# Optimization experiments

Hardware: AMD Instinct MI355X
Metric: run time of the kernel (lower is better)

Reference implementation:

```python
import jax, jax.numpy as jnp
import numpy as np

N_HEAD = 16
ROPE_BASE = 10000.0


def _rope_cache(T, head_dim):
    # half-split RoPE: cos/sin of shape [T, head_dim//2]
    half = head_dim // 2
    inv_freq = ROPE_BASE ** (-jnp.arange(half, dtype=jnp.float32) / half)
    angles = jnp.arange(T, dtype=jnp.float32)[:, None] * inv_freq[None, :]  # [T, half]
    return jnp.cos(angles), jnp.sin(angles)


def _apply_rope(x, cos, sin):
    # x: [B, H, T, D]; cos/sin: [T, D//2]
    half = x.shape[-1] // 2
    x1, x2 = x[..., :half], x[..., half:]
    c = cos[None, None, :, :]
    s = sin[None, None, :, :]
    return jnp.concatenate([x1 * c - x2 * s, x1 * s + x2 * c], axis=-1)


def setup_inputs() -> dict:
    key = jax.random.key(0)
    k1, k2, k3 = jax.random.split(key, 3)
    B, T, C = 2, 2048, 1024
    x = jax.random.normal(k1, (B, T, C), dtype=jnp.float32)
    w_attn = jax.random.normal(k2, (C, 3 * C), dtype=jnp.float32) * (C ** -0.5)
    b_attn = jnp.zeros((3 * C,), dtype=jnp.float32)
    w_proj = jax.random.normal(k3, (C, C), dtype=jnp.float32) * (C ** -0.5)
    b_proj = jnp.zeros((C,), dtype=jnp.float32)
    return {"x": x, "w_attn": w_attn, "b_attn": b_attn, "w_proj": w_proj, "b_proj": b_proj}


def reference(x, w_attn, b_attn, w_proj, b_proj):
    B, T, C = x.shape
    H = N_HEAD
    hd = C // H

    qkv = x @ w_attn + b_attn                      # [B, T, 3C] fused QKV
    q, k, v = jnp.split(qkv, 3, axis=-1)
    q = q.reshape(B, T, H, hd).transpose(0, 2, 1, 3)  # [B, H, T, hd]
    k = k.reshape(B, T, H, hd).transpose(0, 2, 1, 3)
    v = v.reshape(B, T, H, hd).transpose(0, 2, 1, 3)

    cos, sin = _rope_cache(T, hd)
    q = _apply_rope(q, cos, sin)
    k = _apply_rope(k, cos, sin)

    scale = 1.0 / jnp.sqrt(jnp.float32(hd))
    att = jnp.einsum("bhqd,bhkd->bhqk", q, k) * scale  # [B, H, T, T]
    causal = jnp.tril(jnp.ones((T, T), dtype=bool))
    att = jnp.where(causal[None, None], att, -jnp.inf)
    att = jax.nn.softmax(att, axis=-1)
    y = jnp.einsum("bhqk,bhkd->bhqd", att, v)          # [B, H, T, hd]
    y = y.transpose(0, 2, 1, 3).reshape(B, T, C)
    return y @ w_proj + b_proj
```

## Files before the change

kernel.cpp:

```cpp
#include <hip/hip_runtime.h>
#include <hip/hip_bf16.h>
#include <cmath>

typedef _Float16 half_t;
typedef half_t half4 __attribute__((ext_vector_type(4)));
typedef half_t half8 __attribute__((ext_vector_type(8)));
typedef float f32x4 __attribute__((ext_vector_type(4)));

#define N_HEADS 16
#define HD      64
#define T_SEQ   2048
#define B_SZ    2
#define C_DIM   1024
#define M_ROWS  (B_SZ * T_SEQ)
#define N_QKV   (3 * C_DIM)
#define QSCALE  0.18033688f

__device__ inline void load_lds16(const half_t* g, half_t* l) {
  __builtin_amdgcn_global_load_lds(
      (const __attribute__((address_space(1))) void*)g,
      (__attribute__((address_space(3))) void*)l, 16, 0, 0);
}

__global__ __launch_bounds__(256) void k_prep(const float* __restrict__ x,
                                              half_t* __restrict__ xb,
                                              const float* __restrict__ wa,
                                              half_t* __restrict__ wT,
                                              const float* __restrict__ wp,
                                              half_t* __restrict__ wpT,
                                              float2* __restrict__ tbl) {
  __shared__ float tile[64][65];
  int bid = blockIdx.x, tid = threadIdx.x;
  if (bid < 4096) {
    int i = (bid * 256 + tid) * 4;
    float4 v = *(const float4*)(x + i);
    half_t o[4] = {(half_t)v.x, (half_t)v.y, (half_t)v.z, (half_t)v.w};
    *(ulong1*)(xb + i) = *(ulong1*)o;
    return;
  }
  if (bid >= 5120) {
    int idx = (bid - 5120) * 256 + tid;
    int t = idx >> 5, j = idx & 31;
    float inv = exp2f(-(float)j * (13.287712379549449f / 32.0f));
    float s, c;
    sincosf((float)t * inv, &s, &c);
    tbl[idx] = make_float2(c, s);
    return;
  }
  const float* in; half_t* out; int K, N, id;
  if (bid < 4864) { id = bid - 4096; in = wa; out = wT;  K = 1024; N = 3072; }
  else            { id = bid - 4864; in = wp; out = wpT; K = 1024; N = 1024; }
  int n0 = (id % (N / 64)) * 64, k0 = (id / (N / 64)) * 64;
  int tx = tid & 63, ty = tid >> 6;
  #pragma unroll
  for (int i = 0; i < 64; i += 4)
    tile[ty + i][tx] = in[(size_t)(k0 + ty + i) * N + n0 + tx];
  __syncthreads();
  #pragma unroll
  for (int i = 0; i < 64; i += 4) {
    int r = ty + i;
    out[(size_t)(n0 + r) * K + k0 + tx] = (half_t)tile[tx][r];
  }
}

template <typename OT, int TN>
__global__ __launch_bounds__(256) void k_gemm(const half_t* __restrict__ A,
                                              const half_t* __restrict__ Bt,
                                              const float* __restrict__ bias,
                                              OT* __restrict__ C,
                                              int M, int N, int K) {
  constexpr int NI = TN / 32;
  __shared__ half_t As[2][128 * 64];
  __shared__ half_t Bs[2][TN * 64];
  int tid = threadIdx.x;
  int wave = tid >> 6, lane = tid & 63;
  int lane15 = lane & 15, quad = lane >> 4;
  int wm = (wave >> 1) * 64, wn = (wave & 1) * (TN / 2);
  int bm0 = blockIdx.y * 128, bn0 = blockIdx.x * TN;
  f32x4 acc[4][NI] = {};

#define G_STAGE(bb, kb)                                                        \
  {                                                                            \
    const half_t* Ag = A + (size_t)bm0 * K + (kb);                             \
    const half_t* Bg = Bt + (size_t)bn0 * K + (kb);                            \
    _Pragma("unroll")                                                          \
    for (int p = 0; p < 4; p++) {                                              \
      int fc = wave * 4 * 64 + p * 64 + lane;                                  \
      int r = fc >> 3, c = (fc & 7) ^ (r & 7);                                 \
      load_lds16(Ag + (size_t)r * K + c * 8, &As[bb][0] + (wave * 4 + p) * 512); \
    }                                                                          \
    _Pragma("unroll")                                                          \
    for (int p = 0; p < NI; p++) {                                             \
      int fc = wave * NI * 64 + p * 64 + lane;                                 \
      int r = fc >> 3, c = (fc & 7) ^ (r & 7);                                 \
      load_lds16(Bg + (size_t)r * K + c * 8, &Bs[bb][0] + (wave * NI + p) * 512); \
    }                                                                          \
  }

  G_STAGE(0, 0);
  int NT = K / 64;
  for (int kt = 0; kt < NT; kt++) {
    __syncthreads();
    if (kt + 1 < NT) G_STAGE((kt + 1) & 1, (kt + 1) * 64);
    const half_t* Asb = &As[kt & 1][0];
    const half_t* Bsb = &Bs[kt & 1][0];
    #pragma unroll
    for (int ks = 0; ks < 2; ks++) {
      half8 af[4], bf[NI];
      #pragma unroll
      for (int i = 0; i < 4; i++) {
        int Ra = wm + i * 16 + lane15;
        af[i] = *(const half8*)(Asb + Ra * 64 + ((ks * 4 + quad) ^ (Ra & 7)) * 8);
      }
      #pragma unroll
      for (int i = 0; i < NI; i++) {
        int Rb = wn + i * 16 + lane15;
        bf[i] = *(const half8*)(Bsb + Rb * 64 + ((ks * 4 + quad) ^ (Rb & 7)) * 8);
      }
      #pragma unroll
      for (int mi = 0; mi < 4; mi++)
        #pragma unroll
        for (int ni = 0; ni < NI; ni++)
          acc[mi][ni] = __builtin_amdgcn_mfma_f32_16x16x32_f16(af[mi], bf[ni], acc[mi][ni], 0, 0, 0);
    }
  }
#undef G_STAGE
  #pragma unroll
  for (int mi = 0; mi < 4; mi++)
    #pragma unroll
    for (int ni = 0; ni < NI; ni++) {
      int n = bn0 + wn + ni * 16 + lane15;
      float bv = bias[n];
      int mrow = bm0 + wm + mi * 16 + quad * 4;
      #pragma unroll
      for (int r = 0; r < 4; r++)
        C[(size_t)(mrow + r) * N + n] = (OT)(acc[mi][ni][r] + bv);
    }
}

__global__ __launch_bounds__(256) void k_gemm_qkv(const half_t* __restrict__ A,
                                                  const half_t* __restrict__ Bt,
                                                  const float* __restrict__ bias,
                                                  const float2* __restrict__ tbl,
                                                  half_t* __restrict__ Qo,
                                                  half_t* __restrict__ Ko,
                                                  half_t* __restrict__ Vo) {
  __shared__ half_t smem[2][16384];
  int tid = threadIdx.x;
  int wave = tid >> 6, lane = tid & 63;
  int lane15 = lane & 15, quad = lane >> 4;
  int wm = (wave >> 1) * 64, wn = (wave & 1) * 64;
  int bm0 = blockIdx.y * 128, bn0 = blockIdx.x * 128;
  f32x4 acc[4][4] = {};

#define QKV_STAGE(bb, kb)                                                      \
  {                                                                            \
    const half_t* Ag = A + (size_t)bm0 * C_DIM + (kb);                         \
    const half_t* Bg = Bt + (size_t)bn0 * C_DIM + (kb);                        \
    _Pragma("unroll")                                                          \
    for (int p = 0; p < 4; p++) {                                              \
      int fc = wave * 4 * 64 + p * 64 + lane;                                  \
      int r = fc >> 3, c = (fc & 7) ^ (r & 7);                                 \
      load_lds16(Ag + (size_t)r * C_DIM + c * 8,                               \
                 &smem[bb][0] + (wave * 4 + p) * 512);                         \
      load_lds16(Bg + (size_t)r * C_DIM + c * 8,                               \
                 &smem[bb][8192] + (wave * 4 + p) * 512);                      \
    }                                                                          \
  }

  QKV_STAGE(0, 0);
  for (int kt = 0; kt < 16; kt++) {
    __syncthreads();
    if (kt < 15) QKV_STAGE((kt + 1) & 1, (kt + 1) * 64);
    const half_t* As = &smem[kt & 1][0];
    const half_t* Bs = &smem[kt & 1][8192];
    #pragma unroll
    for (int ks = 0; ks < 2; ks++) {
      half8 af[4], bf[4];
      #pragma unroll
      for (int i = 0; i < 4; i++) {
        int Ra = wm + i * 16 + lane15;
        af[i] = *(const half8*)(As + Ra * 64 + ((ks * 4 + quad) ^ (Ra & 7)) * 8);
      }
      #pragma unroll
      for (int i = 0; i < 4; i++) {
        int Rb = wn + i * 16 + lane15;
        bf[i] = *(const half8*)(Bs + Rb * 64 + ((ks * 4 + quad) ^ (Rb & 7)) * 8);
      }
      #pragma unroll
      for (int mi = 0; mi < 4; mi++)
        #pragma unroll
        for (int ni = 0; ni < 4; ni++)
          acc[mi][ni] = __builtin_amdgcn_mfma_f32_16x16x32_f16(af[mi], bf[ni], acc[mi][ni], 0, 0, 0);
    }
  }
#undef QKV_STAGE
  #pragma unroll
  for (int ni = 0; ni < 4; ni++) {
    float bv = bias[bn0 + wn + ni * 16 + lane15];
    #pragma unroll
    for (int mi = 0; mi < 4; mi++)
      #pragma unroll
      for (int r = 0; r < 4; r++) acc[mi][ni][r] += bv;
  }

  int third = bn0 >> 10;
  if (third < 2) {
    half_t* Ob = (third == 0) ? Qo : Ko;
    int h = ((bn0 & 1023) + wn) >> 6;
    #pragma unroll
    for (int mi = 0; mi < 4; mi++) {
      int mrow = bm0 + wm + mi * 16 + quad * 4;
      int bq = mrow >> 11, tq = mrow & 2047;
      half_t* outp = Ob + ((size_t)(bq * 16 + h) * T_SEQ + tq) * HD;
      #pragma unroll
      for (int p = 0; p < 2; p++) {
        int j = p * 16 + lane15;
        #pragma unroll
        for (int r = 0; r < 4; r++) {
          float2 cs = tbl[(tq + r) * 32 + j];
          float a1 = acc[mi][p][r], a2 = acc[mi][p + 2][r];
          float o1 = a1 * cs.x - a2 * cs.y;
          float o2 = a1 * cs.y + a2 * cs.x;
          if (third == 0) { o1 *= QSCALE; o2 *= QSCALE; }
          outp[r * HD + j]      = (half_t)o1;
          outp[r * HD + j + 32] = (half_t)o2;
        }
      }
    }
  } else {
    __syncthreads();
    half_t* vt = &smem[0][0];
    #pragma unroll
    for (int mi = 0; mi < 4; mi++)
      #pragma unroll
      for (int ni = 0; ni < 4; ni++) {
        int tl = wm + mi * 16 + quad * 4, nl = wn + ni * 16 + lane15;
        #pragma unroll
        for (int r = 0; r < 4; r++)
          vt[(tl + r) * 130 + nl] = (half_t)acc[mi][ni][r];
      }
    __syncthreads();
    int hV = (bn0 - 2048) >> 6;
    int bq = bm0 >> 11, tq0 = bm0 & 2047;
    int c8 = (tid & 7) * 8;
    #pragma unroll
    for (int p = 0; p < 8; p++) {
      int gr = p * 32 + (tid >> 3);
      int tb = gr & 1, d = (gr >> 1) & 63, h2 = gr >> 7;
      half8 vv;
      #pragma unroll
      for (int jj = 0; jj < 8; jj++)
        vv[jj] = vt[(tb * 64 + c8 + jj) * 130 + h2 * 64 + d];
      *(half8*)(Vo + ((size_t)((bq * 16 + hV + h2) * 32 + (tq0 >> 6) + tb) * 64 + d) * 64 + c8) = vv;
    }
  }
}

template <bool DIAG>
__device__ __forceinline__ void tile_mfma(const half_t* __restrict__ Kt,
                                          const half_t* __restrict__ Vt,
                                          half8 bq0, half8 bq1,
                                          f32x4 (&ot)[4], float& l,
                                          int lane15, int quad, int qloc) {
  f32x4 sacc[4];
  #pragma unroll
  for (int s = 0; s < 4; s++) {
    int R_ = s * 16 + lane15;
    half8 ak0 = *(const half8*)(Kt + R_ * 64 + ((quad) ^ (R_ & 7)) * 8);
    half8 ak1 = *(const half8*)(Kt + R_ * 64 + ((4 + quad) ^ (R_ & 7)) * 8);
    f32x4 z = {};
    z = __builtin_amdgcn_mfma_f32_16x16x32_f16(ak0, bq0, z, 0, 0, 0);
    sacc[s] = __builtin_amdgcn_mfma_f32_16x16x32_f16(ak1, bq1, z, 0, 0, 0);
  }
  #pragma unroll
  for (int s = 0; s < 4; s++) {
    half4 bp;
    #pragma unroll
    for (int r = 0; r < 4; r++) {
      float sv = sacc[s][r];
      if (DIAG && (s * 16 + quad * 4 + r > qloc)) sv = -1.0e30f;
      float p = exp2f(fminf(sv, 14.0f));
      l += p;
      bp[r] = (half_t)p;
    }
    #pragma unroll
    for (int nm = 0; nm < 4; nm++) {
      int Rv = nm * 16 + lane15;
      half4 av = *(const half4*)(Vt + Rv * 64 +
                                 ((2 * s + (quad >> 1)) ^ (Rv & 7)) * 8 +
                                 (quad & 1) * 4);
      ot[nm] = __builtin_amdgcn_mfma_f32_16x16x16f16(av, bp, ot[nm], 0, 0, 0);
    }
  }
}

#define STAGE(bb, t_)                                                          \
  {                                                                            \
    int gS = wave >> 3;                                                        \
    int idx = (wave & 7) * 64 + lane;                                          \
    int rr_ = idx >> 3, cc = (idx & 7) ^ (rr_ & 7);                            \
    int j = 2 * (t_) + gS;                                                     \
    load_lds16(Kb + (size_t)(j * 64 + rr_) * HD + cc * 8,                      \
               &KV[bb][0][gS][0] + idx * 8);                                   \
    load_lds16(Vb + (size_t)j * 4096 + rr_ * 64 + cc * 8,                      \
               &KV[bb][1][gS][0] + idx * 8);                                   \
  }

__device__ __forceinline__ void process_tile(
    int qt, const half_t* __restrict__ Qb, const half_t* __restrict__ Kb,
    const half_t* __restrict__ Vb, half_t* __restrict__ y, int b, int h,
    half_t (&KV)[2][2][2][4096],
    int wave, int lane, int g, int wq, int lane15, int quad) {
  int q0 = qt * 128;
  int qrow = q0 + wq * 16 + lane15;
  half8 bq0 = *(const half8*)(Qb + (size_t)qrow * HD + quad * 8);
  half8 bq1 = *(const half8*)(Qb + (size_t)qrow * HD + 32 + quad * 8);
  f32x4 ot[4] = {};
  float l = 0.f;
  int R = qt + 1;
  for (int r = 0; r < R - 1; r++) {
    __syncthreads();
    STAGE((r + 1) & 1, r + 1);
    tile_mfma<false>(&KV[r & 1][0][g][0], &KV[r & 1][1][g][0], bq0, bq1, ot, l,
                     lane15, quad, 0);
  }
  __syncthreads();
  {
    int buf = (R - 1) & 1;
    const half_t* Kt = &KV[buf][0][g][0];
    const half_t* Vt = &KV[buf][1][g][0];
    if (g == 0)
      tile_mfma<true>(Kt, Vt, bq0, bq1, ot, l, lane15, quad, wq * 16 + lane15);
    else if (wq >= 4)
      tile_mfma<true>(Kt, Vt, bq0, bq1, ot, l, lane15, quad,
                      (wq - 4) * 16 + lane15);
  }
  l += __shfl_xor(l, 16);
  l += __shfl_xor(l, 32);
  __syncthreads();
  float* cb = (float*)&KV[0][0][0][0];
  int ci = (wq * 64 + lane) * 17;
  if (g == 1) {
    #pragma unroll
    for (int nm = 0; nm < 4; nm++)
      #pragma unroll
      for (int r = 0; r < 4; r++) cb[ci + nm * 4 + r] = ot[nm][r];
    cb[ci + 16] = l;
  }
  __syncthreads();
  if (g == 0) {
    #pragma unroll
    for (int nm = 0; nm < 4; nm++)
      #pragma unroll
      for (int r = 0; r < 4; r++) ot[nm][r] += cb[ci + nm * 4 + r];
    l += cb[ci + 16];
    float invl = 1.0f / l;
    int t = q0 + wq * 16 + lane15;
    half_t* yr = y + (size_t)(b * T_SEQ + t) * C_DIM + h * 64;
    #pragma unroll
    for (int nm = 0; nm < 4; nm++) {
      half4 o4;
      #pragma unroll
      for (int r = 0; r < 4; r++) o4[r] = (half_t)(ot[nm][r] * invl);
      *(half4*)(yr + nm * 16 + quad * 4) = o4;
    }
  }
  __syncthreads();
}

__global__ __launch_bounds__(1024, 4) void k_flash(const half_t* __restrict__ Qg,
                                                   const half_t* __restrict__ Kg,
                                                   const half_t* __restrict__ Vg,
                                                   half_t* __restrict__ y) {
  __shared__ half_t KV[2][2][2][4096];
  int bh = blockIdx.y;
  int b = bh >> 4, h = bh & 15;
  int x = blockIdx.x;
  int tid = threadIdx.x;
  int wave = tid >> 6, lane = tid & 63;
  int g = wave >> 3, wq = wave & 7;
  int lane15 = lane & 15, quad = lane >> 4;
  const half_t* Qb = Qg + (size_t)bh * T_SEQ * HD;
  const half_t* Kb = Kg + (size_t)bh * T_SEQ * HD;
  const half_t* Vb = Vg + (size_t)bh * HD * T_SEQ;

  int qtA = x, qtB = 15 - x;
  STAGE(0, 0);
  process_tile(qtA, Qb, Kb, Vb, y, b, h, KV, wave, lane, g, wq, lane15, quad);
  STAGE(0, 0);
  process_tile(qtB, Qb, Kb, Vb, y, b, h, KV, wave, lane, g, wq, lane15, quad);
  #undef STAGE
}

extern "C" void kernel_launch(void* const* d_in, const int* in_sizes, int n_in,
                              void* d_out, int out_size, void* d_ws, size_t ws_size,
                              hipStream_t stream) {
  const float* x      = (const float*)d_in[0];
  const float* w_attn = (const float*)d_in[1];
  const float* b_attn = (const float*)d_in[2];
  const float* w_proj = (const float*)d_in[3];
  const float* b_proj = (const float*)d_in[4];
  float* out = (float*)d_out;

  char* ws = (char*)d_ws;
  const size_t MB = 1u << 20;
  half_t* xb  = (half_t*)(ws);
  half_t* wT  = (half_t*)(ws + 8 * MB);
  half_t* wpT = (half_t*)(ws + 14 * MB);
  half_t* Q   = (half_t*)(ws + 16 * MB);
  half_t* Kb  = (half_t*)(ws + 24 * MB);
  half_t* Vt  = (half_t*)(ws + 32 * MB);
  half_t* y   = (half_t*)(ws + 40 * MB);
  float2* tbl = (float2*)(ws + 48 * MB);

  k_prep<<<4096 + 768 + 256 + 256, 256, 0, stream>>>(x, xb, w_attn, wT,
                                                     w_proj, wpT, tbl);
  k_gemm_qkv<<<dim3(N_QKV / 128, M_ROWS / 128), 256, 0, stream>>>(
      xb, wT, b_attn, tbl, Q, Kb, Vt);
  k_flash<<<dim3(8, B_SZ * N_HEADS), 1024, 0, stream>>>(Q, Kb, Vt, y);
  k_gemm<float, 64><<<dim3(C_DIM / 64, M_ROWS / 128), 256, 0, stream>>>(
      y, wpT, b_proj, out, M_ROWS, C_DIM, C_DIM);
}
```

Measured before the change: 184.2 us.

## Share K/V tile loads across paired query tiles and remap block indices

The flash kernel used to handle its two query tiles (x and 15-x) one after the other, restaging K/V from the start for the second tile. It now runs a single loop over the longer tile's K/V range and applies each staged K/V tile to both query blocks, so the shared prefix is loaded and synchronized once. Block indices are also remapped so that consecutive blocks cover different heads. The cost is a second set of accumulators per wave, which raises register pressure and may lower occupancy under the 1024-thread launch bound.

```diff
diff --git a/kernel.cpp b/kernel.cpp
--- a/kernel.cpp
+++ b/kernel.cpp
@@ -307,76 +307,15 @@
                &KV[bb][1][gS][0] + idx * 8);                                   \
   }
 
-__device__ __forceinline__ void process_tile(
-    int qt, const half_t* __restrict__ Qb, const half_t* __restrict__ Kb,
-    const half_t* __restrict__ Vb, half_t* __restrict__ y, int b, int h,
-    half_t (&KV)[2][2][2][4096],
-    int wave, int lane, int g, int wq, int lane15, int quad) {
-  int q0 = qt * 128;
-  int qrow = q0 + wq * 16 + lane15;
-  half8 bq0 = *(const half8*)(Qb + (size_t)qrow * HD + quad * 8);
-  half8 bq1 = *(const half8*)(Qb + (size_t)qrow * HD + 32 + quad * 8);
-  f32x4 ot[4] = {};
-  float l = 0.f;
-  int R = qt + 1;
-  for (int r = 0; r < R - 1; r++) {
-    __syncthreads();
-    STAGE((r + 1) & 1, r + 1);
-    tile_mfma<false>(&KV[r & 1][0][g][0], &KV[r & 1][1][g][0], bq0, bq1, ot, l,
-                     lane15, quad, 0);
-  }
-  __syncthreads();
-  {
-    int buf = (R - 1) & 1;
-    const half_t* Kt = &KV[buf][0][g][0];
-    const half_t* Vt = &KV[buf][1][g][0];
-    if (g == 0)
-      tile_mfma<true>(Kt, Vt, bq0, bq1, ot, l, lane15, quad, wq * 16 + lane15);
-    else if (wq >= 4)
-      tile_mfma<true>(Kt, Vt, bq0, bq1, ot, l, lane15, quad,
-                      (wq - 4) * 16 + lane15);
-  }
-  l += __shfl_xor(l, 16);
-  l += __shfl_xor(l, 32);
-  __syncthreads();
-  float* cb = (float*)&KV[0][0][0][0];
-  int ci = (wq * 64 + lane) * 17;
-  if (g == 1) {
-    #pragma unroll
-    for (int nm = 0; nm < 4; nm++)
-      #pragma unroll
-      for (int r = 0; r < 4; r++) cb[ci + nm * 4 + r] = ot[nm][r];
-    cb[ci + 16] = l;
-  }
-  __syncthreads();
-  if (g == 0) {
-    #pragma unroll
-    for (int nm = 0; nm < 4; nm++)
-      #pragma unroll
-      for (int r = 0; r < 4; r++) ot[nm][r] += cb[ci + nm * 4 + r];
-    l += cb[ci + 16];
-    float invl = 1.0f / l;
-    int t = q0 + wq * 16 + lane15;
-    half_t* yr = y + (size_t)(b * T_SEQ + t) * C_DIM + h * 64;
-    #pragma unroll
-    for (int nm = 0; nm < 4; nm++) {
-      half4 o4;
-      #pragma unroll
-      for (int r = 0; r < 4; r++) o4[r] = (half_t)(ot[nm][r] * invl);
-      *(half4*)(yr + nm * 16 + quad * 4) = o4;
-    }
-  }
-  __syncthreads();
-}
-
 __global__ __launch_bounds__(1024, 4) void k_flash(const half_t* __restrict__ Qg,
                                                    const half_t* __restrict__ Kg,
                                                    const half_t* __restrict__ Vg,
                                                    half_t* __restrict__ y) {
   __shared__ half_t KV[2][2][2][4096];
-  int bh = blockIdx.y;
+  int flat = (int)blockIdx.x + 8 * (int)blockIdx.y;
+  int x  = (flat >> 3) & 7;
+  int bh = (flat & 7) | ((flat >> 6) << 3);
   int b = bh >> 4, h = bh & 15;
-  int x = blockIdx.x;
   int tid = threadIdx.x;
   int wave = tid >> 6, lane = tid & 63;
   int g = wave >> 3, wq = wave & 7;
@@ -386,10 +325,97 @@
   const half_t* Vb = Vg + (size_t)bh * HD * T_SEQ;
 
   int qtA = x, qtB = 15 - x;
+  int jA = 2 * qtA, jB = 2 * qtB;
+  int qlA = qtA * 128 + wq * 16 + lane15;
+  int qlB = qtB * 128 + wq * 16 + lane15;
+  half8 aq0 = *(const half8*)(Qb + (size_t)qlA * HD + quad * 8);
+  half8 aq1 = *(const half8*)(Qb + (size_t)qlA * HD + 32 + quad * 8);
+  half8 bq0 = *(const half8*)(Qb + (size_t)qlB * HD + quad * 8);
+  half8 bq1 = *(const half8*)(Qb + (size_t)qlB * HD + 32 + quad * 8);
+  f32x4 otA[4] = {}, otB[4] = {};
+  float lA = 0.f, lB = 0.f;
+
+  int R = 16 - x;
   STAGE(0, 0);
-  process_tile(qtA, Qb, Kb, Vb, y, b, h, KV, wave, lane, g, wq, lane15, quad);
-  STAGE(0, 0);
-  process_tile(qtB, Qb, Kb, Vb, y, b, h, KV, wave, lane, g, wq, lane15, quad);
+  for (int r = 0; r < R; r++) {
+    __syncthreads();
+    if (r + 1 < R) STAGE((r + 1) & 1, r + 1);
+    const half_t* Kt = &KV[r & 1][0][g][0];
+    const half_t* Vt = &KV[r & 1][1][g][0];
+    int j = 2 * r + g;
+    if (j < jA)
+      tile_mfma<false>(Kt, Vt, aq0, aq1, otA, lA, lane15, quad, 0);
+    else if (j == jA)
+      tile_mfma<true>(Kt, Vt, aq0, aq1, otA, lA, lane15, quad,
+                      wq * 16 + lane15);
+    else if (j == jA + 1 && wq >= 4)
+      tile_mfma<true>(Kt, Vt, aq0, aq1, otA, lA, lane15, quad,
+                      (wq - 4) * 16 + lane15);
+    if (j < jB)
+      tile_mfma<false>(Kt, Vt, bq0, bq1, otB, lB, lane15, quad, 0);
+    else if (j == jB)
+      tile_mfma<true>(Kt, Vt, bq0, bq1, otB, lB, lane15, quad,
+                      wq * 16 + lane15);
+    else if (j == jB + 1 && wq >= 4)
+      tile_mfma<true>(Kt, Vt, bq0, bq1, otB, lB, lane15, quad,
+                      (wq - 4) * 16 + lane15);
+  }
+  lA += __shfl_xor(lA, 16); lA += __shfl_xor(lA, 32);
+  lB += __shfl_xor(lB, 16); lB += __shfl_xor(lB, 32);
+  float* cb = (float*)&KV[0][0][0][0];
+  int ci = (wq * 64 + lane) * 17;
+  __syncthreads();
+  if (g == 1) {
+    #pragma unroll
+    for (int nm = 0; nm < 4; nm++)
+      #pragma unroll
+      for (int r = 0; r < 4; r++) cb[ci + nm * 4 + r] = otA[nm][r];
+    cb[ci + 16] = lA;
+  }
+  __syncthreads();
+  if (g == 0) {
+    #pragma unroll
+    for (int nm = 0; nm < 4; nm++)
+      #pragma unroll
+      for (int r = 0; r < 4; r++) otA[nm][r] += cb[ci + nm * 4 + r];
+    lA += cb[ci + 16];
+    float invl = 1.0f / lA;
+    int t = qtA * 128 + wq * 16 + lane15;
+    half_t* yr = y + (size_t)(b * T_SEQ + t) * C_DIM + h * 64;
+    #pragma unroll
+    for (int nm = 0; nm < 4; nm++) {
+      half4 o4;
+      #pragma unroll
+      for (int r = 0; r < 4; r++) o4[r] = (half_t)(otA[nm][r] * invl);
+      *(half4*)(yr + nm * 16 + quad * 4) = o4;
+    }
+  }
+  __syncthreads();
+  if (g == 1) {
+    #pragma unroll
+    for (int nm = 0; nm < 4; nm++)
+      #pragma unroll
+      for (int r = 0; r < 4; r++) cb[ci + nm * 4 + r] = otB[nm][r];
+    cb[ci + 16] = lB;
+  }
+  __syncthreads();
+  if (g == 0) {
+    #pragma unroll
+    for (int nm = 0; nm < 4; nm++)
+      #pragma unroll
+      for (int r = 0; r < 4; r++) otB[nm][r] += cb[ci + nm * 4 + r];
+    lB += cb[ci + 16];
+    float invl = 1.0f / lB;
+    int t = qtB * 128 + wq * 16 + lane15;
+    half_t* yr = y + (size_t)(b * T_SEQ + t) * C_DIM + h * 64;
+    #pragma unroll
+    for (int nm = 0; nm < 4; nm++) {
+      half4 o4;
+      #pragma unroll
+      for (int r = 0; r < 4; r++) o4[r] = (half_t)(otB[nm][r] * invl);
+      *(half4*)(yr + nm * 16 + quad * 4) = o4;
+    }
+  }
   #undef STAGE
 }
 
```

Result: no change. 183.5 us (-0.3%).
